# Kernel optimization log

Hardware: AMD Instinct MI355X
Metric: run time of the kernel (lower is better)

## Reference

```python
import jax, jax.numpy as jnp
import numpy as np


def setup_inputs() -> dict:
    key = jax.random.key(0)
    k1, k2 = jax.random.split(key)
    bg = jax.random.normal(k1, (1, 4, 32, 32, 32, 16), dtype=jnp.float32)
    gm = jax.random.uniform(k2, (1, 1, 128, 128, 128), dtype=jnp.float32)
    return {"bg": bg, "gm": gm}


def _prep(coord, size):
    # replicate boundary: clamp sample coords into [0, size-1]
    coord = jnp.clip(coord, 0.0, float(size - 1))
    i0f = jnp.floor(coord)
    frac = coord - i0f
    i0 = i0f.astype(jnp.int32)
    i1 = jnp.minimum(i0 + 1, size - 1)
    return i0, i1, frac


def reference(bg, gm):
    # bg: (n,c,h,w,d,up) 4D bilateral grid; gm: (n,1,gh,gw,gd) guidance volume
    n, c, h, w, d, up = bg.shape
    _, _, gh, gw, gd = gm.shape
    f32 = jnp.float32

    # voxel-space sample coordinates (module: hg/(h_img-1) * (h-1) etc.)
    x = jnp.arange(gh, dtype=f32) * (f32(h - 1) / f32(gh - 1))  # (gh,)
    y = jnp.arange(gw, dtype=f32) * (f32(w - 1) / f32(gw - 1))  # (gw,)
    z = jnp.arange(gd, dtype=f32) * (f32(d - 1) / f32(gd - 1))  # (gd,)
    t = gm[:, 0] * f32(up - 1)                                   # (n,gh,gw,gd)

    x0, x1, fx = _prep(x, h)
    y0, y1, fy = _prep(y, w)
    z0, z1, fz = _prep(z, d)
    t0, t1, ft = _prep(t, up)

    def opts(i0, i1, frac, shape):
        i0 = i0.reshape(shape); i1 = i1.reshape(shape); frac = frac.reshape(shape)
        return [(i0, 1.0 - frac), (i1, frac)]

    xo = opts(x0, x1, fx, (1, gh, 1, 1))
    yo = opts(y0, y1, fy, (1, 1, gw, 1))
    zo = opts(z0, z1, fz, (1, 1, 1, gd))
    to = [(t0, 1.0 - ft), (t1, ft)]  # already (n,gh,gw,gd)

    bidx = jnp.arange(n)[:, None, None, None]        # (n,1,1,1)
    bgc = jnp.moveaxis(bg, 1, -1)                    # (n,h,w,d,up,c)

    acc = jnp.zeros((n, gh, gw, gd, c), dtype=bg.dtype)
    # 2^4 = 16 corners of quadri-linear interpolation (grid_pull order=1)
    for ix, wx in xo:
        for iy, wy in yo:
            for iz, wz in zo:
                for it, wt in to:
                    vals = bgc[bidx, ix, iy, iz, it]         # (n,gh,gw,gd,c)
                    wgt = (wx * wy * wz * wt)[..., None]     # (n,gh,gw,gd,1)
                    acc = acc + vals * wgt
    return jnp.moveaxis(acc, -1, 1)                  # (n,c,gh,gw,gd)
```

## Files before the change

### kernel.cpp

```cpp
#include <hip/hip_runtime.h>
#include <hip/hip_fp16.h>


#define S_ (31.0f / 127.0f)
#define CH_STRIDE 524288
#define TOTAL 2097152

#define NX 4
#define NY 4
#define NZ 6
#define NNODES (NX * NY * NZ)
#define NODE_DW 68
#define LDS_DW (NNODES * NODE_DW)

__global__ __launch_bounds__(256, 5) void bgrid_slice_v4(
    const float* __restrict__ bg,
    const float* __restrict__ gm,
    float* __restrict__ out)
{
    __shared__ __align__(16) float lds[LDS_DW];

    const int tid = threadIdx.x;
    const int b = blockIdx.x;
    const int bk = b & 7;
    const int bj = (b >> 3) & 15;
    const int bi = b >> 7;

    const int i0 = bi * 8, j0 = bj * 8, k0 = bk * 16;
    const int x_base = (int)((float)i0 * S_);
    const int y_base = (int)((float)j0 * S_);
    const int z_base = (int)((float)k0 * S_);

    for (int q = tid; q < NNODES * 16; q += 256) {
        const int node = q >> 4;
        const int s = q & 15;
        const int a = node / (NY * NZ);
        const int rem = node - a * (NY * NZ);
        const int bb = rem / NZ;
        const int cz = rem - bb * NZ;
        const int gx = min(x_base + a, 31);
        const int gy = min(y_base + bb, 31);
        const int gz = min(z_base + cz, 31);
        const int gbase = (((gx * 32 + gy) * 32 + gz) << 4) + s;

        const float c0 = bg[gbase];
        const float c1 = bg[gbase + CH_STRIDE];
        const float c2 = bg[gbase + 2 * CH_STRIDE];
        const float c3 = bg[gbase + 3 * CH_STRIDE];

        float2 pk;
        pk.x = __builtin_bit_cast(float, __floats2half2_rn(c0, c1));
        pk.y = __builtin_bit_cast(float, __floats2half2_rn(c2, c3));

        const int nb = node * NODE_DW;
        *(float2*)&lds[nb + (s << 2)] = pk;
        if (s > 0)  *(float2*)&lds[nb + ((s - 1) << 2) + 2] = pk;
        if (s == 15) *(float2*)&lds[nb + (15 << 2) + 2] = pk;
    }
    __syncthreads();

    const int kq = tid & 3;
    const int lj = (tid >> 2) & 7;
    const int li = tid >> 5;
    const int i = i0 + li, j = j0 + lj;
    const int kk = k0 + (kq << 2);

    const float xf = fminf((float)i * S_, 31.0f);
    const float yf = fminf((float)j * S_, 31.0f);
    const int x0g = (int)xf; const float fx = xf - (float)x0g;
    const int y0g = (int)yf; const float fy = yf - (float)y0g;
    const int xi0 = x0g - x_base, xi1 = min(x0g + 1, 31) - x_base;
    const int yi0 = y0g - y_base, yi1 = min(y0g + 1, 31) - y_base;

    const int AX0 = xi0 * (NY * NZ * NODE_DW);
    const int AX1 = xi1 * (NY * NZ * NODE_DW);
    const int BY0 = yi0 * (NZ * NODE_DW);
    const int BY1 = yi1 * (NZ * NODE_DW);

    const float wx1 = fx, wx0 = 1.0f - fx;
    const float wy1 = fy, wy0 = 1.0f - fy;
    const __half2 W00 = __float2half2_rn(wx0 * wy0);
    const __half2 W01 = __float2half2_rn(wx0 * wy1);
    const __half2 W10 = __float2half2_rn(wx1 * wy0);
    const __half2 W11 = __float2half2_rn(wx1 * wy1);

    const int idx = (i << 14) | (j << 7) | kk;
    const float4 g4 = *(const float4*)&gm[idx];

    float o0[4], o1[4], o2[4], o3[4];

#pragma unroll
    for (int v = 0; v < 4; ++v) {
        const float g = (v == 0) ? g4.x : (v == 1) ? g4.y : (v == 2) ? g4.z : g4.w;
        float t = fminf(fmaxf(g * 15.0f, 0.0f), 15.0f);
        const int t0 = min((int)t, 14);
        const float ft = t - (float)t0;
        const __half2 ft2 = __float2half2_rn(ft);

        const float zf = fminf((float)(kk + v) * S_, 31.0f);
        const int z0g = (int)zf;
        const float fz = zf - (float)z0g;
        const int zi0 = z0g - z_base;
        const int zi1 = min(z0g + 1, 31) - z_base;
        const __half2 fz2 = __float2half2_rn(fz);

        const int CZ0 = zi0 * NODE_DW + (t0 << 2);
        const int CZ1 = zi1 * NODE_DW + (t0 << 2);

        const float4 a00 = *(const float4*)&lds[AX0 + BY0 + CZ0];
        const float4 a01 = *(const float4*)&lds[AX0 + BY1 + CZ0];
        const float4 a10 = *(const float4*)&lds[AX1 + BY0 + CZ0];
        const float4 a11 = *(const float4*)&lds[AX1 + BY1 + CZ0];
        const float4 b00 = *(const float4*)&lds[AX0 + BY0 + CZ1];
        const float4 b01 = *(const float4*)&lds[AX0 + BY1 + CZ1];
        const float4 b10 = *(const float4*)&lds[AX1 + BY0 + CZ1];
        const float4 b11 = *(const float4*)&lds[AX1 + BY1 + CZ1];

#define H2(f) __builtin_bit_cast(__half2, f)
        __half2 Plo01 = __hmul2(W00, H2(a00.x));
        __half2 Plo23 = __hmul2(W00, H2(a00.y));
        __half2 Phi01 = __hmul2(W00, H2(a00.z));
        __half2 Phi23 = __hmul2(W00, H2(a00.w));
        Plo01 = __hfma2(W01, H2(a01.x), Plo01);
        Plo23 = __hfma2(W01, H2(a01.y), Plo23);
        Phi01 = __hfma2(W01, H2(a01.z), Phi01);
        Phi23 = __hfma2(W01, H2(a01.w), Phi23);
        Plo01 = __hfma2(W10, H2(a10.x), Plo01);
        Plo23 = __hfma2(W10, H2(a10.y), Plo23);
        Phi01 = __hfma2(W10, H2(a10.z), Phi01);
        Phi23 = __hfma2(W10, H2(a10.w), Phi23);
        Plo01 = __hfma2(W11, H2(a11.x), Plo01);
        Plo23 = __hfma2(W11, H2(a11.y), Plo23);
        Phi01 = __hfma2(W11, H2(a11.z), Phi01);
        Phi23 = __hfma2(W11, H2(a11.w), Phi23);

        __half2 Qlo01 = __hmul2(W00, H2(b00.x));
        __half2 Qlo23 = __hmul2(W00, H2(b00.y));
        __half2 Qhi01 = __hmul2(W00, H2(b00.z));
        __half2 Qhi23 = __hmul2(W00, H2(b00.w));
        Qlo01 = __hfma2(W01, H2(b01.x), Qlo01);
        Qlo23 = __hfma2(W01, H2(b01.y), Qlo23);
        Qhi01 = __hfma2(W01, H2(b01.z), Qhi01);
        Qhi23 = __hfma2(W01, H2(b01.w), Qhi23);
        Qlo01 = __hfma2(W10, H2(b10.x), Qlo01);
        Qlo23 = __hfma2(W10, H2(b10.y), Qlo23);
        Qhi01 = __hfma2(W10, H2(b10.z), Qhi01);
        Qhi23 = __hfma2(W10, H2(b10.w), Qhi23);
        Qlo01 = __hfma2(W11, H2(b11.x), Qlo01);
        Qlo23 = __hfma2(W11, H2(b11.y), Qlo23);
        Qhi01 = __hfma2(W11, H2(b11.z), Qhi01);
        Qhi23 = __hfma2(W11, H2(b11.w), Qhi23);
#undef H2

        const __half2 Rlo01 = __hfma2(fz2, __hsub2(Qlo01, Plo01), Plo01);
        const __half2 Rlo23 = __hfma2(fz2, __hsub2(Qlo23, Plo23), Plo23);
        const __half2 Rhi01 = __hfma2(fz2, __hsub2(Qhi01, Plo01 ), Phi01);
        const __half2 Rhi23 = __hfma2(fz2, __hsub2(Qhi23, Phi23), Phi23);
        const __half2 Rhi01f = __hfma2(fz2, __hsub2(Qhi01, Phi01), Phi01);

        const __half2 r01 = __hfma2(ft2, __hsub2(Rhi01f, Rlo01), Rlo01);
        const __half2 r23 = __hfma2(ft2, __hsub2(Rhi23, Rlo23), Rlo23);
        (void)Rhi01;

        o0[v] = __low2float(r01);
        o1[v] = __high2float(r01);
        o2[v] = __low2float(r23);
        o3[v] = __high2float(r23);
    }

    float4 st;
    st.x = o0[0]; st.y = o0[1]; st.z = o0[2]; st.w = o0[3];
    *(float4*)&out[idx] = st;
    st.x = o1[0]; st.y = o1[1]; st.z = o1[2]; st.w = o1[3];
    *(float4*)&out[idx + TOTAL] = st;
    st.x = o2[0]; st.y = o2[1]; st.z = o2[2]; st.w = o2[3];
    *(float4*)&out[idx + 2 * TOTAL] = st;
    st.x = o3[0]; st.y = o3[1]; st.z = o3[2]; st.w = o3[3];
    *(float4*)&out[idx + 3 * TOTAL] = st;
}

extern "C" void kernel_launch(void* const* d_in, const int* in_sizes, int n_in,
                              void* d_out, int out_size, void* d_ws, size_t ws_size,
                              hipStream_t stream) {
    const float* bg = (const float*)d_in[0];
    const float* gm = (const float*)d_in[1];
    float* out = (float*)d_out;

    dim3 grid(2048);
    dim3 block(256);
    bgrid_slice_v4<<<grid, block, 0, stream>>>(bg, gm, out);
}
```

Measured before the change: 19.53 us.

## Pre-pack grid into fp16 node layout in workspace, stage via direct global-to-LDS loads

Adds a repack kernel that converts the bilateral grid into a per-node fp16 packed layout with duplicated neighbour pairs in a workspace buffer. The slice kernel then fills LDS with 16-byte global_load_lds transfers instead of per-thread gather, convert and scatter, and it remaps block IDs to change tile ordering across CUs. It also cleans up the z-interpolation arithmetic and keeps the old kernel as a fallback when the workspace is too small. The trade-off is an extra kernel launch and an extra full pass over the grid each call.

```diff
diff --git a/kernel.cpp b/kernel.cpp
--- a/kernel.cpp
+++ b/kernel.cpp
@@ -10,11 +10,36 @@
 #define NY 4
 #define NZ 6
 #define NNODES (NX * NY * NZ)
-#define NODE_DW 68
+#define NODE_DW 64
 #define LDS_DW (NNODES * NODE_DW)
-
-__global__ __launch_bounds__(256, 5) void bgrid_slice_v4(
-    const float* __restrict__ bg,
+#define WS_BYTES (32768 * 256)
+
+typedef __attribute__((address_space(3))) void lds_void_t;
+typedef const __attribute__((address_space(1))) void gbl_void_t;
+
+__global__ __launch_bounds__(256) void bgrid_repack(
+    const float* __restrict__ bg, float* __restrict__ ws)
+{
+    const int u = blockIdx.x * 256 + threadIdx.x;
+    const int s = u & 15;
+
+    const float c0 = bg[u];
+    const float c1 = bg[u + CH_STRIDE];
+    const float c2 = bg[u + 2 * CH_STRIDE];
+    const float c3 = bg[u + 3 * CH_STRIDE];
+
+    float2 pk;
+    pk.x = __builtin_bit_cast(float, __floats2half2_rn(c0, c1));
+    pk.y = __builtin_bit_cast(float, __floats2half2_rn(c2, c3));
+
+    const int nb = (u >> 4) << 6;
+    const int sl = nb + (s << 2);
+    *(float2*)&ws[sl] = pk;
+    if (s > 0) *(float2*)&ws[sl - 2] = pk;
+}
+
+__global__ __launch_bounds__(256) void bgrid_slice_v5(
+    const float* __restrict__ ws,
     const float* __restrict__ gm,
     float* __restrict__ out)
 {
@@ -22,40 +47,31 @@
 
     const int tid = threadIdx.x;
     const int b = blockIdx.x;
-    const int bk = b & 7;
-    const int bj = (b >> 3) & 15;
-    const int bi = b >> 7;
+    const int tile = ((b & 7) << 8) + (b >> 3);
+    const int bk = tile & 7;
+    const int bj = (tile >> 3) & 15;
+    const int bi = tile >> 7;
 
     const int i0 = bi * 8, j0 = bj * 8, k0 = bk * 16;
     const int x_base = (int)((float)i0 * S_);
     const int y_base = (int)((float)j0 * S_);
     const int z_base = (int)((float)k0 * S_);
 
-    for (int q = tid; q < NNODES * 16; q += 256) {
-        const int node = q >> 4;
+    const char* wsb = (const char*)ws;
+    #pragma unroll
+    for (int it = 0; it < 6; ++it) {
+        const int q = tid + it * 256;
+        const int n = q >> 4;
         const int s = q & 15;
-        const int a = node / (NY * NZ);
-        const int rem = node - a * (NY * NZ);
+        const int a = n / (NY * NZ);
+        const int rem = n - a * (NY * NZ);
         const int bb = rem / NZ;
         const int cz = rem - bb * NZ;
         const int gx = min(x_base + a, 31);
         const int gy = min(y_base + bb, 31);
         const int gz = min(z_base + cz, 31);
-        const int gbase = (((gx * 32 + gy) * 32 + gz) << 4) + s;
-
-        const float c0 = bg[gbase];
-        const float c1 = bg[gbase + CH_STRIDE];
-        const float c2 = bg[gbase + 2 * CH_STRIDE];
-        const float c3 = bg[gbase + 3 * CH_STRIDE];
-
-        float2 pk;
-        pk.x = __builtin_bit_cast(float, __floats2half2_rn(c0, c1));
-        pk.y = __builtin_bit_cast(float, __floats2half2_rn(c2, c3));
-
-        const int nb = node * NODE_DW;
-        *(float2*)&lds[nb + (s << 2)] = pk;
-        if (s > 0)  *(float2*)&lds[nb + ((s - 1) << 2) + 2] = pk;
-        if (s == 15) *(float2*)&lds[nb + (15 << 2) + 2] = pk;
+        gbl_void_t* src = (gbl_void_t*)(wsb + ((((gx * 32 + gy) * 32 + gz) << 8) + (s << 4)));
+        __builtin_amdgcn_global_load_lds(src, (lds_void_t*)&lds[q << 2], 16, 0, 0);
     }
     __syncthreads();
 
@@ -154,13 +170,11 @@
 
         const __half2 Rlo01 = __hfma2(fz2, __hsub2(Qlo01, Plo01), Plo01);
         const __half2 Rlo23 = __hfma2(fz2, __hsub2(Qlo23, Plo23), Plo23);
-        const __half2 Rhi01 = __hfma2(fz2, __hsub2(Qhi01, Plo01 ), Phi01);
+        const __half2 Rhi01 = __hfma2(fz2, __hsub2(Qhi01, Phi01), Phi01);
         const __half2 Rhi23 = __hfma2(fz2, __hsub2(Qhi23, Phi23), Phi23);
-        const __half2 Rhi01f = __hfma2(fz2, __hsub2(Qhi01, Phi01), Phi01);
-
-        const __half2 r01 = __hfma2(ft2, __hsub2(Rhi01f, Rlo01), Rlo01);
+
+        const __half2 r01 = __hfma2(ft2, __hsub2(Rhi01, Rlo01), Rlo01);
         const __half2 r23 = __hfma2(ft2, __hsub2(Rhi23, Rlo23), Rlo23);
-        (void)Rhi01;
 
         o0[v] = __low2float(r01);
         o1[v] = __high2float(r01);
@@ -179,6 +193,171 @@
     *(float4*)&out[idx + 3 * TOTAL] = st;
 }
 
+#define FNODE_DW 68
+__global__ __launch_bounds__(256, 5) void bgrid_slice_fb(
+    const float* __restrict__ bg,
+    const float* __restrict__ gm,
+    float* __restrict__ out)
+{
+    __shared__ __align__(16) float lds[NNODES * FNODE_DW];
+
+    const int tid = threadIdx.x;
+    const int b = blockIdx.x;
+    const int bk = b & 7;
+    const int bj = (b >> 3) & 15;
+    const int bi = b >> 7;
+
+    const int i0 = bi * 8, j0 = bj * 8, k0 = bk * 16;
+    const int x_base = (int)((float)i0 * S_);
+    const int y_base = (int)((float)j0 * S_);
+    const int z_base = (int)((float)k0 * S_);
+
+    for (int q = tid; q < NNODES * 16; q += 256) {
+        const int node = q >> 4;
+        const int s = q & 15;
+        const int a = node / (NY * NZ);
+        const int rem = node - a * (NY * NZ);
+        const int bb = rem / NZ;
+        const int cz = rem - bb * NZ;
+        const int gx = min(x_base + a, 31);
+        const int gy = min(y_base + bb, 31);
+        const int gz = min(z_base + cz, 31);
+        const int gbase = (((gx * 32 + gy) * 32 + gz) << 4) + s;
+
+        const float c0 = bg[gbase];
+        const float c1 = bg[gbase + CH_STRIDE];
+        const float c2 = bg[gbase + 2 * CH_STRIDE];
+        const float c3 = bg[gbase + 3 * CH_STRIDE];
+
+        float2 pk;
+        pk.x = __builtin_bit_cast(float, __floats2half2_rn(c0, c1));
+        pk.y = __builtin_bit_cast(float, __floats2half2_rn(c2, c3));
+
+        const int nb = node * FNODE_DW;
+        *(float2*)&lds[nb + (s << 2)] = pk;
+        if (s > 0)  *(float2*)&lds[nb + ((s - 1) << 2) + 2] = pk;
+        if (s == 15) *(float2*)&lds[nb + (15 << 2) + 2] = pk;
+    }
+    __syncthreads();
+
+    const int kq = tid & 3;
+    const int lj = (tid >> 2) & 7;
+    const int li = tid >> 5;
+    const int i = i0 + li, j = j0 + lj;
+    const int kk = k0 + (kq << 2);
+
+    const float xf = fminf((float)i * S_, 31.0f);
+    const float yf = fminf((float)j * S_, 31.0f);
+    const int x0g = (int)xf; const float fx = xf - (float)x0g;
+    const int y0g = (int)yf; const float fy = yf - (float)y0g;
+    const int xi0 = x0g - x_base, xi1 = min(x0g + 1, 31) - x_base;
+    const int yi0 = y0g - y_base, yi1 = min(y0g + 1, 31) - y_base;
+
+    const int AX0 = xi0 * (NY * NZ * FNODE_DW);
+    const int AX1 = xi1 * (NY * NZ * FNODE_DW);
+    const int BY0 = yi0 * (NZ * FNODE_DW);
+    const int BY1 = yi1 * (NZ * FNODE_DW);
+
+    const float wx1 = fx, wx0 = 1.0f - fx;
+    const float wy1 = fy, wy0 = 1.0f - fy;
+    const __half2 W00 = __float2half2_rn(wx0 * wy0);
+    const __half2 W01 = __float2half2_rn(wx0 * wy1);
+    const __half2 W10 = __float2half2_rn(wx1 * wy0);
+    const __half2 W11 = __float2half2_rn(wx1 * wy1);
+
+    const int idx = (i << 14) | (j << 7) | kk;
+    const float4 g4 = *(const float4*)&gm[idx];
+
+    float o0[4], o1[4], o2[4], o3[4];
+
+#pragma unroll
+    for (int v = 0; v < 4; ++v) {
+        const float g = (v == 0) ? g4.x : (v == 1) ? g4.y : (v == 2) ? g4.z : g4.w;
+        float t = fminf(fmaxf(g * 15.0f, 0.0f), 15.0f);
+        const int t0 = min((int)t, 14);
+        const float ft = t - (float)t0;
+        const __half2 ft2 = __float2half2_rn(ft);
+
+        const float zf = fminf((float)(kk + v) * S_, 31.0f);
+        const int z0g = (int)zf;
+        const float fz = zf - (float)z0g;
+        const int zi0 = z0g - z_base;
+        const int zi1 = min(z0g + 1, 31) - z_base;
+        const __half2 fz2 = __float2half2_rn(fz);
+
+        const int CZ0 = zi0 * FNODE_DW + (t0 << 2);
+        const int CZ1 = zi1 * FNODE_DW + (t0 << 2);
+
+        const float4 a00 = *(const float4*)&lds[AX0 + BY0 + CZ0];
+        const float4 a01 = *(const float4*)&lds[AX0 + BY1 + CZ0];
+        const float4 a10 = *(const float4*)&lds[AX1 + BY0 + CZ0];
+        const float4 a11 = *(const float4*)&lds[AX1 + BY1 + CZ0];
+        const float4 b00 = *(const float4*)&lds[AX0 + BY0 + CZ1];
+        const float4 b01 = *(const float4*)&lds[AX0 + BY1 + CZ1];
+        const float4 b10 = *(const float4*)&lds[AX1 + BY0 + CZ1];
+        const float4 b11 = *(const float4*)&lds[AX1 + BY1 + CZ1];
+
+#define H2(f) __builtin_bit_cast(__half2, f)
+        __half2 Plo01 = __hmul2(W00, H2(a00.x));
+        __half2 Plo23 = __hmul2(W00, H2(a00.y));
+        __half2 Phi01 = __hmul2(W00, H2(a00.z));
+        __half2 Phi23 = __hmul2(W00, H2(a00.w));
+        Plo01 = __hfma2(W01, H2(a01.x), Plo01);
+        Plo23 = __hfma2(W01, H2(a01.y), Plo23);
+        Phi01 = __hfma2(W01, H2(a01.z), Phi01);
+        Phi23 = __hfma2(W01, H2(a01.w), Phi23);
+        Plo01 = __hfma2(W10, H2(a10.x), Plo01);
+        Plo23 = __hfma2(W10, H2(a10.y), Plo23);
+        Phi01 = __hfma2(W10, H2(a10.z), Phi01);
+        Phi23 = __hfma2(W10, H2(a10.w), Phi23);
+        Plo01 = __hfma2(W11, H2(a11.x), Plo01);
+        Plo23 = __hfma2(W11, H2(a11.y), Plo23);
+        Phi01 = __hfma2(W11, H2(a11.z), Phi01);
+        Phi23 = __hfma2(W11, H2(a11.w), Phi23);
+
+        __half2 Qlo01 = __hmul2(W00, H2(b00.x));
+        __half2 Qlo23 = __hmul2(W00, H2(b00.y));
+        __half2 Qhi01 = __hmul2(W00, H2(b00.z));
+        __half2 Qhi23 = __hmul2(W00, H2(b00.w));
+        Qlo01 = __hfma2(W01, H2(b01.x), Qlo01);
+        Qlo23 = __hfma2(W01, H2(b01.y), Qlo23);
+        Qhi01 = __hfma2(W01, H2(b01.z), Qhi01);
+        Qhi23 = __hfma2(W01, H2(b01.w), Qhi23);
+        Qlo01 = __hfma2(W10, H2(b10.x), Qlo01);
+        Qlo23 = __hfma2(W10, H2(b10.y), Qlo23);
+        Qhi01 = __hfma2(W10, H2(b10.z), Qhi01);
+        Qhi23 = __hfma2(W10, H2(b10.w), Qhi23);
+        Qlo01 = __hfma2(W11, H2(b11.x), Qlo01);
+        Qlo23 = __hfma2(W11, H2(b11.y), Qlo23);
+        Qhi01 = __hfma2(W11, H2(b11.z), Qhi01);
+        Qhi23 = __hfma2(W11, H2(b11.w), Qhi23);
+#undef H2
+
+        const __half2 Rlo01 = __hfma2(fz2, __hsub2(Qlo01, Plo01), Plo01);
+        const __half2 Rlo23 = __hfma2(fz2, __hsub2(Qlo23, Plo23), Plo23);
+        const __half2 Rhi01 = __hfma2(fz2, __hsub2(Qhi01, Phi01), Phi01);
+        const __half2 Rhi23 = __hfma2(fz2, __hsub2(Qhi23, Phi23), Phi23);
+
+        const __half2 r01 = __hfma2(ft2, __hsub2(Rhi01, Rlo01), Rlo01);
+        const __half2 r23 = __hfma2(ft2, __hsub2(Rhi23, Rlo23), Rlo23);
+
+        o0[v] = __low2float(r01);
+        o1[v] = __high2float(r01);
+        o2[v] = __low2float(r23);
+        o3[v] = __high2float(r23);
+    }
+
+    float4 st;
+    st.x = o0[0]; st.y = o0[1]; st.z = o0[2]; st.w = o0[3];
+    *(float4*)&out[idx] = st;
+    st.x = o1[0]; st.y = o1[1]; st.z = o1[2]; st.w = o1[3];
+    *(float4*)&out[idx + TOTAL] = st;
+    st.x = o2[0]; st.y = o2[1]; st.z = o2[2]; st.w = o2[3];
+    *(float4*)&out[idx + 2 * TOTAL] = st;
+    st.x = o3[0]; st.y = o3[1]; st.z = o3[2]; st.w = o3[3];
+    *(float4*)&out[idx + 3 * TOTAL] = st;
+}
+
 extern "C" void kernel_launch(void* const* d_in, const int* in_sizes, int n_in,
                               void* d_out, int out_size, void* d_ws, size_t ws_size,
                               hipStream_t stream) {
@@ -186,7 +365,11 @@
     const float* gm = (const float*)d_in[1];
     float* out = (float*)d_out;
 
-    dim3 grid(2048);
-    dim3 block(256);
-    bgrid_slice_v4<<<grid, block, 0, stream>>>(bg, gm, out);
+    if (ws_size >= (size_t)WS_BYTES) {
+        float* ws = (float*)d_ws;
+        bgrid_repack<<<dim3(2048), dim3(256), 0, stream>>>(bg, ws);
+        bgrid_slice_v5<<<dim3(2048), dim3(256), 0, stream>>>(ws, gm, out);
+    } else {
+        bgrid_slice_fb<<<dim3(2048), dim3(256), 0, stream>>>(bg, gm, out);
+    }
 }
```

Result: slower. 24.74 us (+26.7%).

## Store each grid node once in LDS, vectorise staging loads, remap tile order

Applied to the files above, without the earlier changes.

Each node's t-slices are now stored once in LDS (36 dwords instead of 68 duplicated pairs), and compute reads two float2 per corner instead of one float4. The staging loop uses float4 global loads covering four t-slices per thread, in place of scalar loads. Blocks are reordered so consecutive blocks step along i/j instead of k, and occupancy is raised to 6 blocks per CU. The smaller LDS footprint allows more resident blocks, at the cost of twice as many LDS read instructions and a different cache locality pattern for grid-node loads.

```diff
diff --git a/kernel.cpp b/kernel.cpp
--- a/kernel.cpp
+++ b/kernel.cpp
@@ -10,10 +10,10 @@
 #define NY 4
 #define NZ 6
 #define NNODES (NX * NY * NZ)
-#define NODE_DW 68
+#define NODE_DW 36
 #define LDS_DW (NNODES * NODE_DW)
 
-__global__ __launch_bounds__(256, 5) void bgrid_slice_v4(
+__global__ __launch_bounds__(256, 6) void bgrid_slice_v7(
     const float* __restrict__ bg,
     const float* __restrict__ gm,
     float* __restrict__ out)
@@ -22,40 +22,47 @@
 
     const int tid = threadIdx.x;
     const int b = blockIdx.x;
-    const int bk = b & 7;
-    const int bj = (b >> 3) & 15;
-    const int bi = b >> 7;
+    const int tile = ((b & 7) << 8) + (b >> 3);
+    const int bk = tile & 7;
+    const int bj = (tile >> 3) & 15;
+    const int bi = tile >> 7;
 
     const int i0 = bi * 8, j0 = bj * 8, k0 = bk * 16;
     const int x_base = (int)((float)i0 * S_);
     const int y_base = (int)((float)j0 * S_);
     const int z_base = (int)((float)k0 * S_);
 
-    for (int q = tid; q < NNODES * 16; q += 256) {
-        const int node = q >> 4;
-        const int s = q & 15;
-        const int a = node / (NY * NZ);
-        const int rem = node - a * (NY * NZ);
-        const int bb = rem / NZ;
-        const int cz = rem - bb * NZ;
-        const int gx = min(x_base + a, 31);
-        const int gy = min(y_base + bb, 31);
-        const int gz = min(z_base + cz, 31);
-        const int gbase = (((gx * 32 + gy) * 32 + gz) << 4) + s;
-
-        const float c0 = bg[gbase];
-        const float c1 = bg[gbase + CH_STRIDE];
-        const float c2 = bg[gbase + 2 * CH_STRIDE];
-        const float c3 = bg[gbase + 3 * CH_STRIDE];
-
-        float2 pk;
-        pk.x = __builtin_bit_cast(float, __floats2half2_rn(c0, c1));
-        pk.y = __builtin_bit_cast(float, __floats2half2_rn(c2, c3));
-
-        const int nb = node * NODE_DW;
-        *(float2*)&lds[nb + (s << 2)] = pk;
-        if (s > 0)  *(float2*)&lds[nb + ((s - 1) << 2) + 2] = pk;
-        if (s == 15) *(float2*)&lds[nb + (15 << 2) + 2] = pk;
+    #pragma unroll
+    for (int it = 0; it < 2; ++it) {
+        const int q = tid + it * 256;
+        if (q < NNODES * 4) {
+            const int s4 = q & 3;
+            const int node = q >> 2;
+            const int a = node / (NY * NZ);
+            const int rem = node - a * (NY * NZ);
+            const int bb = rem / NZ;
+            const int cz = rem - bb * NZ;
+            const int gx = min(x_base + a, 31);
+            const int gy = min(y_base + bb, 31);
+            const int gz = min(z_base + cz, 31);
+            const int gbase = (((gx * 32 + gy) * 32 + gz) << 4) + (s4 << 2);
+
+            const float4 L0 = *(const float4*)&bg[gbase];
+            const float4 L1 = *(const float4*)&bg[gbase + CH_STRIDE];
+            const float4 L2 = *(const float4*)&bg[gbase + 2 * CH_STRIDE];
+            const float4 L3 = *(const float4*)&bg[gbase + 3 * CH_STRIDE];
+
+#define PK(x, y) __builtin_bit_cast(float, __floats2half2_rn((x), (y)))
+            float4 W0, W1;
+            W0.x = PK(L0.x, L1.x); W0.y = PK(L2.x, L3.x);
+            W0.z = PK(L0.y, L1.y); W0.w = PK(L2.y, L3.y);
+            W1.x = PK(L0.z, L1.z); W1.y = PK(L2.z, L3.z);
+            W1.z = PK(L0.w, L1.w); W1.w = PK(L2.w, L3.w);
+#undef PK
+            const int d = node * NODE_DW + (s4 << 3);
+            *(float4*)&lds[d] = W0;
+            *(float4*)&lds[d + 4] = W1;
+        }
     }
     __syncthreads();
 
@@ -89,6 +96,7 @@
 
     float o0[4], o1[4], o2[4], o3[4];
 
+#define H2(f) __builtin_bit_cast(__half2, f)
 #pragma unroll
     for (int v = 0; v < 4; ++v) {
         const float g = (v == 0) ? g4.x : (v == 1) ? g4.y : (v == 2) ? g4.z : g4.w;
@@ -104,69 +112,74 @@
         const int zi1 = min(z0g + 1, 31) - z_base;
         const __half2 fz2 = __float2half2_rn(fz);
 
-        const int CZ0 = zi0 * NODE_DW + (t0 << 2);
-        const int CZ1 = zi1 * NODE_DW + (t0 << 2);
-
-        const float4 a00 = *(const float4*)&lds[AX0 + BY0 + CZ0];
-        const float4 a01 = *(const float4*)&lds[AX0 + BY1 + CZ0];
-        const float4 a10 = *(const float4*)&lds[AX1 + BY0 + CZ0];
-        const float4 a11 = *(const float4*)&lds[AX1 + BY1 + CZ0];
-        const float4 b00 = *(const float4*)&lds[AX0 + BY0 + CZ1];
-        const float4 b01 = *(const float4*)&lds[AX0 + BY1 + CZ1];
-        const float4 b10 = *(const float4*)&lds[AX1 + BY0 + CZ1];
-        const float4 b11 = *(const float4*)&lds[AX1 + BY1 + CZ1];
-
-#define H2(f) __builtin_bit_cast(__half2, f)
-        __half2 Plo01 = __hmul2(W00, H2(a00.x));
-        __half2 Plo23 = __hmul2(W00, H2(a00.y));
-        __half2 Phi01 = __hmul2(W00, H2(a00.z));
-        __half2 Phi23 = __hmul2(W00, H2(a00.w));
-        Plo01 = __hfma2(W01, H2(a01.x), Plo01);
-        Plo23 = __hfma2(W01, H2(a01.y), Plo23);
-        Phi01 = __hfma2(W01, H2(a01.z), Phi01);
-        Phi23 = __hfma2(W01, H2(a01.w), Phi23);
-        Plo01 = __hfma2(W10, H2(a10.x), Plo01);
-        Plo23 = __hfma2(W10, H2(a10.y), Plo23);
-        Phi01 = __hfma2(W10, H2(a10.z), Phi01);
-        Phi23 = __hfma2(W10, H2(a10.w), Phi23);
-        Plo01 = __hfma2(W11, H2(a11.x), Plo01);
-        Plo23 = __hfma2(W11, H2(a11.y), Plo23);
-        Phi01 = __hfma2(W11, H2(a11.z), Phi01);
-        Phi23 = __hfma2(W11, H2(a11.w), Phi23);
-
-        __half2 Qlo01 = __hmul2(W00, H2(b00.x));
-        __half2 Qlo23 = __hmul2(W00, H2(b00.y));
-        __half2 Qhi01 = __hmul2(W00, H2(b00.z));
-        __half2 Qhi23 = __hmul2(W00, H2(b00.w));
-        Qlo01 = __hfma2(W01, H2(b01.x), Qlo01);
-        Qlo23 = __hfma2(W01, H2(b01.y), Qlo23);
-        Qhi01 = __hfma2(W01, H2(b01.z), Qhi01);
-        Qhi23 = __hfma2(W01, H2(b01.w), Qhi23);
-        Qlo01 = __hfma2(W10, H2(b10.x), Qlo01);
-        Qlo23 = __hfma2(W10, H2(b10.y), Qlo23);
-        Qhi01 = __hfma2(W10, H2(b10.z), Qhi01);
-        Qhi23 = __hfma2(W10, H2(b10.w), Qhi23);
-        Qlo01 = __hfma2(W11, H2(b11.x), Qlo01);
-        Qlo23 = __hfma2(W11, H2(b11.y), Qlo23);
-        Qhi01 = __hfma2(W11, H2(b11.z), Qhi01);
-        Qhi23 = __hfma2(W11, H2(b11.w), Qhi23);
-#undef H2
+        const int CZ0 = zi0 * NODE_DW + (t0 << 1);
+        const int CZ1 = zi1 * NODE_DW + (t0 << 1);
+
+        const float2 a00lo = *(const float2*)&lds[AX0 + BY0 + CZ0];
+        const float2 a00hi = *(const float2*)&lds[AX0 + BY0 + CZ0 + 2];
+        const float2 a01lo = *(const float2*)&lds[AX0 + BY1 + CZ0];
+        const float2 a01hi = *(const float2*)&lds[AX0 + BY1 + CZ0 + 2];
+        const float2 a10lo = *(const float2*)&lds[AX1 + BY0 + CZ0];
+        const float2 a10hi = *(const float2*)&lds[AX1 + BY0 + CZ0 + 2];
+        const float2 a11lo = *(const float2*)&lds[AX1 + BY1 + CZ0];
+        const float2 a11hi = *(const float2*)&lds[AX1 + BY1 + CZ0 + 2];
+        const float2 b00lo = *(const float2*)&lds[AX0 + BY0 + CZ1];
+        const float2 b00hi = *(const float2*)&lds[AX0 + BY0 + CZ1 + 2];
+        const float2 b01lo = *(const float2*)&lds[AX0 + BY1 + CZ1];
+        const float2 b01hi = *(const float2*)&lds[AX0 + BY1 + CZ1 + 2];
+        const float2 b10lo = *(const float2*)&lds[AX1 + BY0 + CZ1];
+        const float2 b10hi = *(const float2*)&lds[AX1 + BY0 + CZ1 + 2];
+        const float2 b11lo = *(const float2*)&lds[AX1 + BY1 + CZ1];
+        const float2 b11hi = *(const float2*)&lds[AX1 + BY1 + CZ1 + 2];
+
+        __half2 Plo01 = __hmul2(W00, H2(a00lo.x));
+        __half2 Plo23 = __hmul2(W00, H2(a00lo.y));
+        __half2 Phi01 = __hmul2(W00, H2(a00hi.x));
+        __half2 Phi23 = __hmul2(W00, H2(a00hi.y));
+        Plo01 = __hfma2(W01, H2(a01lo.x), Plo01);
+        Plo23 = __hfma2(W01, H2(a01lo.y), Plo23);
+        Phi01 = __hfma2(W01, H2(a01hi.x), Phi01);
+        Phi23 = __hfma2(W01, H2(a01hi.y), Phi23);
+        Plo01 = __hfma2(W10, H2(a10lo.x), Plo01);
+        Plo23 = __hfma2(W10, H2(a10lo.y), Plo23);
+        Phi01 = __hfma2(W10, H2(a10hi.x), Phi01);
+        Phi23 = __hfma2(W10, H2(a10hi.y), Phi23);
+        Plo01 = __hfma2(W11, H2(a11lo.x), Plo01);
+        Plo23 = __hfma2(W11, H2(a11lo.y), Plo23);
+        Phi01 = __hfma2(W11, H2(a11hi.x), Phi01);
+        Phi23 = __hfma2(W11, H2(a11hi.y), Phi23);
+
+        __half2 Qlo01 = __hmul2(W00, H2(b00lo.x));
+        __half2 Qlo23 = __hmul2(W00, H2(b00lo.y));
+        __half2 Qhi01 = __hmul2(W00, H2(b00hi.x));
+        __half2 Qhi23 = __hmul2(W00, H2(b00hi.y));
+        Qlo01 = __hfma2(W01, H2(b01lo.x), Qlo01);
+        Qlo23 = __hfma2(W01, H2(b01lo.y), Qlo23);
+        Qhi01 = __hfma2(W01, H2(b01hi.x), Qhi01);
+        Qhi23 = __hfma2(W01, H2(b01hi.y), Qhi23);
+        Qlo01 = __hfma2(W10, H2(b10lo.x), Qlo01);
+        Qlo23 = __hfma2(W10, H2(b10lo.y), Qlo23);
+        Qhi01 = __hfma2(W10, H2(b10hi.x), Qhi01);
+        Qhi23 = __hfma2(W10, H2(b10hi.y), Qhi23);
+        Qlo01 = __hfma2(W11, H2(b11lo.x), Qlo01);
+        Qlo23 = __hfma2(W11, H2(b11lo.y), Qlo23);
+        Qhi01 = __hfma2(W11, H2(b11hi.x), Qhi01);
+        Qhi23 = __hfma2(W11, H2(b11hi.y), Qhi23);
 
         const __half2 Rlo01 = __hfma2(fz2, __hsub2(Qlo01, Plo01), Plo01);
         const __half2 Rlo23 = __hfma2(fz2, __hsub2(Qlo23, Plo23), Plo23);
-        const __half2 Rhi01 = __hfma2(fz2, __hsub2(Qhi01, Plo01 ), Phi01);
+        const __half2 Rhi01 = __hfma2(fz2, __hsub2(Qhi01, Phi01), Phi01);
         const __half2 Rhi23 = __hfma2(fz2, __hsub2(Qhi23, Phi23), Phi23);
-        const __half2 Rhi01f = __hfma2(fz2, __hsub2(Qhi01, Phi01), Phi01);
-
-        const __half2 r01 = __hfma2(ft2, __hsub2(Rhi01f, Rlo01), Rlo01);
+
+        const __half2 r01 = __hfma2(ft2, __hsub2(Rhi01, Rlo01), Rlo01);
         const __half2 r23 = __hfma2(ft2, __hsub2(Rhi23, Rlo23), Rlo23);
-        (void)Rhi01;
 
         o0[v] = __low2float(r01);
         o1[v] = __high2float(r01);
         o2[v] = __low2float(r23);
         o3[v] = __high2float(r23);
     }
+#undef H2
 
     float4 st;
     st.x = o0[0]; st.y = o0[1]; st.z = o0[2]; st.w = o0[3];
@@ -188,5 +201,5 @@
 
     dim3 grid(2048);
     dim3 block(256);
-    bgrid_slice_v4<<<grid, block, 0, stream>>>(bg, gm, out);
+    bgrid_slice_v7<<<grid, block, 0, stream>>>(bg, gm, out);
 }
```

New measurement: 21.03 us. 1.08x slower.
